# Performance work log

Hardware: AMD Instinct MI355X
Metric: run time of the kernel (lower is better)

## Reference

```python
import jax, jax.numpy as jnp
import numpy as np

N, N_BINS = 100000, 512
BATCH, K = 8192, 16


def setup_inputs() -> dict:
    key = jax.random.key(0)
    k1, k2, k3 = jax.random.split(key, 3)
    outputs = jax.random.uniform(k1, (N, N_BINS), dtype=jnp.float32)
    # y holds (float-encoded) neighbor indices; trunc(y) must index rows of outputs
    y = jax.random.randint(k2, (BATCH, K), 0, N).astype(jnp.float32)
    weights = jax.random.uniform(k3, (BATCH,), dtype=jnp.float32)
    return {"outputs": outputs, "y": y, "weights": weights}


def reference(outputs, y, weights):
    n, n_bins = outputs.shape
    batch_size, k = y.shape
    nns = jnp.trunc(y).astype(jnp.int32)  # (B, k) indices into outputs rows

    # Torch builds add[a,b,c] = outputs[nns[c,a], b] + outputs[c, b] with shape
    # (k, n_bins, batch) then maxes over bins. Equivalent, batch-major layout:
    o_nn = outputs[nns]  # (B, k, n_bins) gather
    add = jnp.max(o_nn + outputs[:batch_size, None, :], axis=-1)  # (B, k)

    booster_weights = jnp.clip((2.0 - jnp.mean(add, axis=1)) / 2.0, 0.5)  # (B,)
    add_mean = jnp.mean(add * weights[:, None])
    diff = jnp.square(2.0 - add_mean)

    target_b = n / n_bins
    b_col = jnp.sum(outputs[:batch_size], axis=0)  # (n_bins,)
    b = jnp.max(b_col) - jnp.min(b_col)

    cost = b / target_b + diff
    return (cost, diff, b / target_b, booster_weights)
```

## Files before the change

### kernel.cpp

```cpp
#include <hip/hip_runtime.h>

#define NBINS 512

__global__ void init_ws_kernel(float* __restrict__ ws, int n) {
    int t = blockIdx.x * blockDim.x + threadIdx.x;
    if (t < n) ws[t] = 0.0f;
}

__global__ __launch_bounds__(1024) void main_kernel(
        const float* __restrict__ outputs,
        const float* __restrict__ y,
        const float* __restrict__ weights,
        float* __restrict__ out,
        float* __restrict__ accum,
        int K) {
    __shared__ float4 sbase[NBINS / 4];
    __shared__ float s_add[16];

    const int b = blockIdx.x;
    const int t = threadIdx.x;

    if (t < NBINS / 4)
        sbase[t] = ((const float4*)(outputs + (size_t)b * NBINS))[t];
    __syncthreads();

    const int w = t >> 6;
    const int lane = t & 63;

    const int nn = (int)y[b * K + w];
    const float4* rp = (const float4*)(outputs + (size_t)nn * NBINS);
    float4 g0 = rp[lane * 2];
    float4 g1 = rp[lane * 2 + 1];
    float4 b0 = sbase[lane * 2];
    float4 b1 = sbase[lane * 2 + 1];

    float m = fmaxf(fmaxf(fmaxf(g0.x + b0.x, g0.y + b0.y),
                          fmaxf(g0.z + b0.z, g0.w + b0.w)),
                    fmaxf(fmaxf(g1.x + b1.x, g1.y + b1.y),
                          fmaxf(g1.z + b1.z, g1.w + b1.w)));

    #pragma unroll
    for (int off = 32; off > 0; off >>= 1)
        m = fmaxf(m, __shfl_down(m, off, 64));

    if (lane == 0) s_add[w] = m;
    __syncthreads();

    if (t == 0) {
        float sum = 0.0f;
        #pragma unroll
        for (int i = 0; i < 16; ++i) sum += s_add[i];
        float mean = sum * (1.0f / 16.0f);
        float booster = fmaxf(0.5f, (2.0f - mean) * 0.5f);
        out[3 + b] = booster;
        atomicAdd(&accum[b & 255], weights[b] * sum);
    }
}

__global__ void colsum_kernel(const float* __restrict__ outputs,
                              float* __restrict__ bcol,
                              int rows_per_block) {
    const int t = threadIdx.x;
    const int r0 = blockIdx.x * rows_per_block;
    float local = 0.0f;
    for (int r = 0; r < rows_per_block; ++r)
        local += outputs[(size_t)(r0 + r) * NBINS + t];
    atomicAdd(&bcol[t], local);
}

__global__ void final_kernel(const float* __restrict__ bcol,
                             const float* __restrict__ accum,
                             float* __restrict__ out,
                             float inv_count, float inv_target) {
    __shared__ float smax[NBINS];
    __shared__ float smin[NBINS];
    const int t = threadIdx.x;
    float v = bcol[t];
    smax[t] = v;
    smin[t] = v;
    __syncthreads();
    for (int s = NBINS / 2; s > 0; s >>= 1) {
        if (t < s) {
            smax[t] = fmaxf(smax[t], smax[t + s]);
            smin[t] = fminf(smin[t], smin[t + s]);
        }
        __syncthreads();
    }
    if (t == 0) {
        float acc = 0.0f;
        for (int i = 0; i < 256; ++i) acc += accum[i];
        float add_mean = acc * inv_count;
        float d = 2.0f - add_mean;
        float diff = d * d;
        float bn = (smax[0] - smin[0]) * inv_target;
        out[0] = bn + diff;
        out[1] = diff;
        out[2] = bn;
    }
}

extern "C" void kernel_launch(void* const* d_in, const int* in_sizes, int n_in,
                              void* d_out, int out_size, void* d_ws, size_t ws_size,
                              hipStream_t stream) {
    const float* outputs = (const float*)d_in[0];
    const float* y       = (const float*)d_in[1];
    const float* weights = (const float*)d_in[2];
    float* out = (float*)d_out;

    const int B = in_sizes[2];
    const int K = in_sizes[1] / B;
    const int N = in_sizes[0] / NBINS;

    float* ws    = (float*)d_ws;
    float* bcol  = ws;
    float* accum = ws + NBINS;

    init_ws_kernel<<<1, 1024, 0, stream>>>(ws, NBINS + 256);

    main_kernel<<<B, K * 64, 0, stream>>>(outputs, y, weights, out, accum, K);

    const int rows_per_block = 128;
    colsum_kernel<<<B / rows_per_block, NBINS, 0, stream>>>(outputs, bcol, rows_per_block);

    final_kernel<<<1, NBINS, 0, stream>>>(bcol, accum, out,
                                          1.0f / (float)(B * K),
                                          (float)NBINS / (float)N);
}
```

Baseline: 324.6 us.

## Process four neighbors per wavefront and drop shared-memory base row staging

Each wavefront now handles four neighbor rows instead of one, so blocks shrink from 1024 to 256 threads. The base row is read directly into registers and reused across the four gathers, which removes the shared-memory staging and one barrier. Neighbor indices are loaded as one float4 per wave. The colsum kernel also uses fewer rows per block and therefore more blocks. The trade-off is higher register pressure in exchange for more independent loads in flight per thread.

```diff
diff --git a/kernel.cpp b/kernel.cpp
--- a/kernel.cpp
+++ b/kernel.cpp
@@ -7,43 +7,72 @@
     if (t < n) ws[t] = 0.0f;
 }
 
-__global__ __launch_bounds__(1024) void main_kernel(
+__global__ __launch_bounds__(256) void main_kernel(
         const float* __restrict__ outputs,
         const float* __restrict__ y,
         const float* __restrict__ weights,
         float* __restrict__ out,
         float* __restrict__ accum,
         int K) {
-    __shared__ float4 sbase[NBINS / 4];
     __shared__ float s_add[16];
 
     const int b = blockIdx.x;
     const int t = threadIdx.x;
-
-    if (t < NBINS / 4)
-        sbase[t] = ((const float4*)(outputs + (size_t)b * NBINS))[t];
-    __syncthreads();
-
     const int w = t >> 6;
     const int lane = t & 63;
 
-    const int nn = (int)y[b * K + w];
-    const float4* rp = (const float4*)(outputs + (size_t)nn * NBINS);
-    float4 g0 = rp[lane * 2];
-    float4 g1 = rp[lane * 2 + 1];
-    float4 b0 = sbase[lane * 2];
-    float4 b1 = sbase[lane * 2 + 1];
+    const float4 yv = ((const float4*)(y + (size_t)b * K))[w];
+    const int nn0 = (int)yv.x;
+    const int nn1 = (int)yv.y;
+    const int nn2 = (int)yv.z;
+    const int nn3 = (int)yv.w;
 
-    float m = fmaxf(fmaxf(fmaxf(g0.x + b0.x, g0.y + b0.y),
-                          fmaxf(g0.z + b0.z, g0.w + b0.w)),
-                    fmaxf(fmaxf(g1.x + b1.x, g1.y + b1.y),
-                          fmaxf(g1.z + b1.z, g1.w + b1.w)));
+    const float4* bp = (const float4*)(outputs + (size_t)b * NBINS);
+    const float4* r0 = (const float4*)(outputs + (size_t)nn0 * NBINS);
+    const float4* r1 = (const float4*)(outputs + (size_t)nn1 * NBINS);
+    const float4* r2 = (const float4*)(outputs + (size_t)nn2 * NBINS);
+    const float4* r3 = (const float4*)(outputs + (size_t)nn3 * NBINS);
+
+    const int i0 = lane * 2;
+    const int i1 = lane * 2 + 1;
+
+    float4 base0 = bp[i0], base1 = bp[i1];
+    float4 a0 = r0[i0], a1 = r0[i1];
+    float4 c0 = r1[i0], c1 = r1[i1];
+    float4 d0 = r2[i0], d1 = r2[i1];
+    float4 e0 = r3[i0], e1 = r3[i1];
+
+    float m0 = fmaxf(fmaxf(fmaxf(a0.x + base0.x, a0.y + base0.y),
+                           fmaxf(a0.z + base0.z, a0.w + base0.w)),
+                     fmaxf(fmaxf(a1.x + base1.x, a1.y + base1.y),
+                           fmaxf(a1.z + base1.z, a1.w + base1.w)));
+    float m1 = fmaxf(fmaxf(fmaxf(c0.x + base0.x, c0.y + base0.y),
+                           fmaxf(c0.z + base0.z, c0.w + base0.w)),
+                     fmaxf(fmaxf(c1.x + base1.x, c1.y + base1.y),
+                           fmaxf(c1.z + base1.z, c1.w + base1.w)));
+    float m2 = fmaxf(fmaxf(fmaxf(d0.x + base0.x, d0.y + base0.y),
+                           fmaxf(d0.z + base0.z, d0.w + base0.w)),
+                     fmaxf(fmaxf(d1.x + base1.x, d1.y + base1.y),
+                           fmaxf(d1.z + base1.z, d1.w + base1.w)));
+    float m3 = fmaxf(fmaxf(fmaxf(e0.x + base0.x, e0.y + base0.y),
+                           fmaxf(e0.z + base0.z, e0.w + base0.w)),
+                     fmaxf(fmaxf(e1.x + base1.x, e1.y + base1.y),
+                           fmaxf(e1.z + base1.z, e1.w + base1.w)));
 
     #pragma unroll
-    for (int off = 32; off > 0; off >>= 1)
-        m = fmaxf(m, __shfl_down(m, off, 64));
+    for (int off = 32; off > 0; off >>= 1) {
+        m0 = fmaxf(m0, __shfl_down(m0, off, 64));
+        m1 = fmaxf(m1, __shfl_down(m1, off, 64));
+        m2 = fmaxf(m2, __shfl_down(m2, off, 64));
+        m3 = fmaxf(m3, __shfl_down(m3, off, 64));
+    }
 
-    if (lane == 0) s_add[w] = m;
+    if (lane == 0) {
+        s_add[w * 4 + 0] = m0;
+        s_add[w * 4 + 1] = m1;
+        s_add[w * 4 + 2] = m2;
+        s_add[w * 4 + 3] = m3;
+    }
     __syncthreads();
 
     if (t == 0) {
@@ -117,9 +146,9 @@
 
     init_ws_kernel<<<1, 1024, 0, stream>>>(ws, NBINS + 256);
 
-    main_kernel<<<B, K * 64, 0, stream>>>(outputs, y, weights, out, accum, K);
+    main_kernel<<<B, (K / 4) * 64, 0, stream>>>(outputs, y, weights, out, accum, K);
 
-    const int rows_per_block = 128;
+    const int rows_per_block = 32;
     colsum_kernel<<<B / rows_per_block, NBINS, 0, stream>>>(outputs, bcol, rows_per_block);
 
     final_kernel<<<1, NBINS, 0, stream>>>(bcol, accum, out,
```

Result: faster. 299.2 us (-7.8%).
